# Kernel optimization log

Hardware: AMD Instinct MI355X
Metric: run time of the kernel (lower is better)

## Reference

```python
import jax, jax.numpy as jnp
import numpy as np

K = 3       # attractive nearest neighbors
J = 3       # repulsive offset (uses dist[:, :, J:])
ALPHA = 0.1
NU = 1e-3


def setup_inputs() -> dict:
    key = jax.random.key(0)
    k1, k2 = jax.random.split(key, 2)
    phi_p = jax.random.normal(k1, (4, 512, 64, 64), dtype=jnp.float32)
    memory_bank = jax.random.normal(k2, (16384, 512), dtype=jnp.float32)
    r = jnp.ones((1,), dtype=jnp.float32)
    return {"phi_p": phi_p, "memory_bank": memory_bank, "r": r}


def reference(phi_p, memory_bank, r):
    B, C, H, W = phi_p.shape
    # b c h w -> b (h w) c
    x = phi_p.reshape(B, C, H * W).transpose(0, 2, 1)
    x2 = jnp.sum(x * x, axis=-1, keepdims=True)            # [B, HW, 1]
    m2 = jnp.sum(memory_bank * memory_bank, axis=-1)       # [N]
    d2 = x2 + m2[None, None, :] - 2.0 * jnp.einsum('bnc,mc->bnm', x, memory_bank)
    d2 = jnp.maximum(d2, 0.0)                              # [B, HW, N]
    # smallest K+J squared distances, ascending (topk(largest=False))
    neg_top, _ = jax.lax.top_k(-d2, K + J)
    dist = -neg_top                                        # [B, HW, K+J]
    r2 = r ** 2
    scores_att = dist[:, :, :K] - r2
    loss_att = jnp.mean(jnp.maximum(scores_att, 0.0)) / NU
    scores_rep = r2 - dist[:, :, J:] - ALPHA
    loss_rep = jnp.mean(jnp.maximum(scores_rep, 0.0)) / NU
    return loss_att + loss_rep
```

## Files before the change

kernel.cpp:

```cpp
#include <hip/hip_runtime.h>
#include <cfloat>

#define B_   4
#define C_   512
#define HW_  4096
#define R_   16384
#define N_   16384
#define ALPHA_ 0.1f
#define SCALE_ ((float)(1000.0/49152.0))

typedef unsigned int u32;
typedef unsigned short u16;
typedef unsigned char u8;
typedef __attribute__((ext_vector_type(2))) unsigned long long u64x2;
typedef __attribute__((ext_vector_type(4))) float f32x4;

typedef const __attribute__((address_space(1))) u32* gas_u32;
typedef __attribute__((address_space(3))) u32* las_u32;

__device__ __forceinline__ void async16(const void* g, void* l) {
    __builtin_amdgcn_global_load_lds((gas_u32)g, (las_u32)l, 16, 0, 0);
}

__device__ __forceinline__ u32 pk_fp8x4(float a, float b, float c, float d) {
    u32 v = __builtin_amdgcn_cvt_pk_fp8_f32(a, b, 0, false);
    v = __builtin_amdgcn_cvt_pk_fp8_f32(c, d, v, true);
    return v;
}

__device__ __forceinline__ void ins6(float (&t)[6], float v) {
    if (v < t[5]) {
        t[5] = v;
        #pragma unroll
        for (int q = 5; q >= 1; --q) {
            float lo = fminf(t[q-1], t[q]);
            float hi = fmaxf(t[q-1], t[q]);
            t[q-1] = lo; t[q] = hi;
        }
    }
}

__global__ void conv_mem_kernel(const float* __restrict__ mem,
                                u8* __restrict__ Mb, float* __restrict__ m2) {
    int w = threadIdx.x >> 6, l = threadIdx.x & 63;
    int row = blockIdx.x * 4 + w;
    const float4* p = (const float4*)(mem + (size_t)row * C_);
    float4 a = p[l], b = p[l + 64];
    float s = a.x*a.x + a.y*a.y + a.z*a.z + a.w*a.w
            + b.x*b.x + b.y*b.y + b.z*b.z + b.w*b.w;
    *(u32*)(Mb + (size_t)row * C_ + l*4)       = pk_fp8x4(a.x, a.y, a.z, a.w);
    *(u32*)(Mb + (size_t)row * C_ + 256 + l*4) = pk_fp8x4(b.x, b.y, b.z, b.w);
    #pragma unroll
    for (int off = 32; off > 0; off >>= 1) s += __shfl_down(s, off);
    if (l == 0) m2[row] = s;
}

__global__ void conv_phi_kernel(const float* __restrict__ phi, u8* __restrict__ Xb,
                                float* __restrict__ x2) {
    __shared__ float T[64][65];
    int t = threadIdx.x;
    int n0 = blockIdx.x * 64, c0 = blockIdx.y * 64, b = blockIdx.z;
    const float* src = phi + ((size_t)b * C_ + c0) * HW_ + n0;
    int l = t & 63, cg = t >> 6;
    float sq = 0.f;
    #pragma unroll
    for (int p = 0; p < 16; ++p) {
        int c = cg + p * 4;
        float v = src[(size_t)c * HW_ + l];
        T[c][l] = v;
        sq = fmaf(v, v, sq);
    }
    atomicAdd(&x2[(size_t)b * HW_ + n0 + l], sq);
    __syncthreads();
    int cq = t & 15, gl0 = t >> 4;
    #pragma unroll
    for (int p = 0; p < 4; ++p) {
        int gl = gl0 + p * 16;
        u32 v = pk_fp8x4(T[cq*4+0][gl], T[cq*4+1][gl],
                         T[cq*4+2][gl], T[cq*4+3][gl]);
        size_t g = (size_t)b * HW_ + n0 + gl;
        *(u32*)(Xb + g * C_ + c0 + cq*4) = v;
    }
}

template<int NC>
__global__ __launch_bounds__(256, 3) void gemm_topk_kernel(
    const u8* __restrict__ Xb, const u8* __restrict__ Mb,
    const float* __restrict__ m2, float* __restrict__ P ) {
    __shared__ __align__(16) u8 smem[32768];
    const int t = threadIdx.x;
    const int w = t >> 6, l = t & 63;
    const int g0  = blockIdx.x * 64;
    const int n0c = blockIdx.y * (N_ / NC);
    const int mband = w * 32;
    const int fm  = l & 15;
    const int rq  = l >> 4;
    const int pc  = (rq ^ ((fm >> 1) & 3)) * 16;
    const int srow4 = l >> 2;
    const int soff  = (((l & 3) ^ ((l >> 3) & 3)) * 16);

    u64x2 ax[4][2];
    {
        const u8* Xr = Xb + (size_t)(g0 + w*16 + fm) * C_ + rq * 16;
        #pragma unroll
        for (int s = 0; s < 4; ++s) {
            ax[s][0] = *(const u64x2*)(Xr + s*128);
            ax[s][1] = *(const u64x2*)(Xr + s*128 + 64);
        }
    }

    float top[4][6];
    #pragma unroll
    for (int s4 = 0; s4 < 4; ++s4)
        #pragma unroll
        for (int q = 0; q < 6; ++q) top[s4][q] = FLT_MAX;

    {
        const u8* Msrc = Mb + (size_t)(n0c + mband) * C_;
        #pragma unroll
        for (int h = 0; h < 2; ++h)
            #pragma unroll
            for (int i = 0; i < 2; ++i)
                async16(Msrc + (size_t)(i*16 + srow4) * C_ + h*64 + soff,
                        smem + mband*64 + h*8192 + i*1024);
    }
    __syncthreads();

    const int NT = N_ / NC / 128;
    #pragma unroll 1
    for (int nt = 0; nt < NT; ++nt) {
        const int n0 = n0c + nt * 128;

        f32x4 acc[8];
        #pragma unroll
        for (int n = 0; n < 8; ++n) acc[n] = (f32x4)0.f;

        #pragma unroll
        for (int s = 0; s < 4; ++s) {
            {
                const int nt2 = (s == 3) ? nt + 1 : nt;
                const int s2  = (s + 1) & 3;
                if (nt2 < NT) {
                    const u8* Msrc = Mb + (size_t)(n0c + nt2*128 + mband) * C_ + s2*128;
                    u8* dst = smem + ((s+1)&1)*16384 + mband*64;
                    #pragma unroll
                    for (int h = 0; h < 2; ++h)
                        #pragma unroll
                        for (int i = 0; i < 2; ++i)
                            async16(Msrc + (size_t)(i*16 + srow4) * C_ + h*64 + soff,
                                    dst + h*8192 + i*1024);
                }
            }
            const u8* bufp = smem + (s&1)*16384;
            #pragma unroll
            for (int h = 0; h < 2; ++h) {
                const u8* Mh = bufp + h * 8192;
                const u64x2 a = ax[s][h];
                #pragma unroll
                for (int n = 0; n < 8; ++n) {
                    u64x2 bv = *(const u64x2*)(Mh + (n*16 + fm) * 64 + pc);
                    acc[n] = __builtin_amdgcn_mfma_f32_16x16x32_fp8_fp8(
                        (long)a.x, (long)bv.x, acc[n], 0, 0, 0);
                    acc[n] = __builtin_amdgcn_mfma_f32_16x16x32_fp8_fp8(
                        (long)a.y, (long)bv.y, acc[n], 0, 0, 0);
                }
            }

            if (s == 3) {
                float m2w[8];
                #pragma unroll
                for (int n = 0; n < 8; ++n) m2w[n] = m2[n0 + n * 16 + fm];
                #pragma unroll
                for (int j = 0; j < 4; ++j) {
                    float d0 = m2w[0] - 2.f * acc[0][j];
                    float d1 = m2w[1] - 2.f * acc[1][j];
                    float d2 = m2w[2] - 2.f * acc[2][j];
                    float d3 = m2w[3] - 2.f * acc[3][j];
                    float d4 = m2w[4] - 2.f * acc[4][j];
                    float d5 = m2w[5] - 2.f * acc[5][j];
                    float d6 = m2w[6] - 2.f * acc[6][j];
                    float d7 = m2w[7] - 2.f * acc[7][j];
                    float vmin = fminf(fminf(fminf(d0, d1), fminf(d2, d3)),
                                       fminf(fminf(d4, d5), fminf(d6, d7)));
                    float (&tt)[6] = top[j];
                    if (vmin < tt[5]) {
                        ins6(tt, d0); ins6(tt, d1); ins6(tt, d2); ins6(tt, d3);
                        ins6(tt, d4); ins6(tt, d5); ins6(tt, d6); ins6(tt, d7);
                    }
                }
            }
            __syncthreads();
        }
    }

    float* Mg = (float*)smem;
    #pragma unroll
    for (int j = 0; j < 4; ++j) {
        int lrow = w * 16 + rq * 4 + j;
        #pragma unroll
        for (int q = 0; q < 6; ++q)
            Mg[lrow * 97 + fm * 6 + q] = top[j][q];
    }
    __syncthreads();
    if (t < 64) {
        float t6[6];
        #pragma unroll
        for (int q = 0; q < 6; ++q) t6[q] = FLT_MAX;
        const float* row = Mg + t * 97;
        for (int v = 0; v < 96; ++v) ins6(t6, row[v]);
        float* dst = P + ((size_t)(g0 + t) * NC + blockIdx.y) * 6;
        #pragma unroll
        for (int q = 0; q < 6; ++q) dst[q] = t6[q];
    }
}

template<int NC>
__global__ void finalize_kernel(const float* __restrict__ P, const float* __restrict__ x2,
                                const float* __restrict__ rp, float* __restrict__ out) {
    int g = blockIdx.x * 256 + threadIdx.x;
    float t6[6];
    #pragma unroll
    for (int q = 0; q < 6; ++q) t6[q] = FLT_MAX;
    const f32x4* pp = (const f32x4*)(P + (size_t)g * (NC * 6));
    #pragma unroll
    for (int q = 0; q < NC * 6 / 4; ++q) {
        f32x4 v = pp[q];
        ins6(t6, v.x); ins6(t6, v.y); ins6(t6, v.z); ins6(t6, v.w);
    }
    float x2g = x2[g];
    float rv = rp[0], r2 = rv * rv;
    float s = 0.f;
    #pragma unroll
    for (int i = 0; i < 3; ++i) {
        float d = fmaxf(t6[i] + x2g, 0.f);
        s += fmaxf(d - r2, 0.f);
    }
    #pragma unroll
    for (int i = 3; i < 6; ++i) {
        float d = fmaxf(t6[i] + x2g, 0.f);
        s += fmaxf(r2 - d - ALPHA_, 0.f);
    }
    #pragma unroll
    for (int off = 32; off > 0; off >>= 1) s += __shfl_down(s, off);
    __shared__ float red[4];
    int w = threadIdx.x >> 6, l = threadIdx.x & 63;
    if (l == 0) red[w] = s;
    __syncthreads();
    if (threadIdx.x == 0)
        atomicAdd(out, (red[0] + red[1] + red[2] + red[3]) * SCALE_);
}

#define TM 64
#define TN 64
#define KC 64
#define LDP 68

__global__ void m2_kernel(const float* __restrict__ mem, float* __restrict__ m2) {
    int wave = threadIdx.x >> 6, lane = threadIdx.x & 63;
    int row = blockIdx.x * 4 + wave;
    const float4* p = reinterpret_cast<const float4*>(mem + (size_t)row * C_);
    float4 a = p[lane], b = p[lane + 64];
    float s = a.x*a.x + a.y*a.y + a.z*a.z + a.w*a.w
            + b.x*b.x + b.y*b.y + b.z*b.z + b.w*b.w;
    #pragma unroll
    for (int off = 32; off > 0; off >>= 1) s += __shfl_down(s, off);
    if (lane == 0) m2[row] = s;
}

__global__ void x2f_kernel(const float* __restrict__ phi, float* __restrict__ x2) {
    int g = blockIdx.x * blockDim.x + threadIdx.x;
    int b = g >> 12;
    int n = g & 4095;
    const float* p = phi + (size_t)b * C_ * HW_ + n;
    float s = 0.f;
    #pragma unroll 8
    for (int c = 0; c < C_; ++c) {
        float v = p[(size_t)c * HW_];
        s = fmaf(v, v, s);
    }
    x2[g] = s;
}

__global__ __launch_bounds__(256) void dist_loss_kernel(
    const float* __restrict__ phi, const float* __restrict__ mem,
    const float* __restrict__ rp,  const float* __restrict__ m2,
    const float* __restrict__ x2,  float* __restrict__ out) {
    __shared__ float smem[2 * TM * LDP];
    float* xs = smem;
    float* ms = smem + TM * LDP;
    const int tid = threadIdx.x;
    const int tx = tid & 15, ty = tid >> 4;
    const int g0 = blockIdx.x * TM;
    const int b = g0 >> 12, n0img = g0 & 4095;
    const float* phiB = phi + (size_t)b * C_ * HW_ + n0img;
    float top[4][6];
    #pragma unroll
    for (int i = 0; i < 4; ++i)
        #pragma unroll
        for (int q = 0; q < 6; ++q) top[i][q] = FLT_MAX;
    float x2v[4];
    #pragma unroll
    for (int i = 0; i < 4; ++i) x2v[i] = x2[g0 + ty * 4 + i];
    for (int nt = 0; nt < N_ / TN; ++nt) {
        const int n0 = nt * TN;
        float acc[4][4];
        #pragma unroll
        for (int i = 0; i < 4; ++i)
            #pragma unroll
            for (int j = 0; j < 4; ++j) acc[i][j] = 0.f;
        for (int s = 0; s < C_ / KC; ++s) {
            const int k0 = s * KC;
            {
                int rr = tid & 63, cb = tid >> 6;
                #pragma unroll
                for (int p = 0; p < 16; ++p) {
                    int cc = p * 4 + cb;
                    xs[rr * LDP + cc] = phiB[(size_t)(k0 + cc) * HW_ + rr];
                }
            }
            {
                int kq = tid & 15, cb = tid >> 4;
                #pragma unroll
                for (int p = 0; p < 4; ++p) {
                    int c = p * 16 + cb;
                    float4 v = *reinterpret_cast<const float4*>(
                        mem + (size_t)(n0 + c) * C_ + k0 + kq * 4);
                    ms[(kq*4+0)*LDP + c] = v.x; ms[(kq*4+1)*LDP + c] = v.y;
                    ms[(kq*4+2)*LDP + c] = v.z; ms[(kq*4+3)*LDP + c] = v.w;
                }
            }
            __syncthreads();
            #pragma unroll
            for (int kq = 0; kq < KC / 4; ++kq) {
                float4 xa[4], mb[4];
                #pragma unroll
                for (int i = 0; i < 4; ++i)
                    xa[i] = *reinterpret_cast<const float4*>(&xs[(ty*4+i)*LDP + kq*4]);
                #pragma unroll
                for (int kk = 0; kk < 4; ++kk)
                    mb[kk] = *reinterpret_cast<const float4*>(&ms[(kq*4+kk)*LDP + tx*4]);
                #pragma unroll
                for (int i = 0; i < 4; ++i) {
                    const float xk[4] = {xa[i].x, xa[i].y, xa[i].z, xa[i].w};
                    #pragma unroll
                    for (int kk = 0; kk < 4; ++kk) {
                        const float mc[4] = {mb[kk].x, mb[kk].y, mb[kk].z, mb[kk].w};
                        #pragma unroll
                        for (int j = 0; j < 4; ++j)
                            acc[i][j] = fmaf(xk[kk], mc[j], acc[i][j]);
                    }
                }
            }
            __syncthreads();
        }
        #pragma unroll
        for (int j = 0; j < 4; ++j) {
            float m2v = m2[n0 + tx * 4 + j];
            #pragma unroll
            for (int i = 0; i < 4; ++i) {
                float d = fmaxf(x2v[i] + m2v - 2.f * acc[i][j], 0.f);
                ins6(top[i], d);
            }
        }
    }
    __syncthreads();
    float* mg = smem;
    #pragma unroll
    for (int i = 0; i < 4; ++i)
        #pragma unroll
        for (int q = 0; q < 6; ++q)
            mg[(ty*4+i)*97 + tx*6 + q] = top[i][q];
    __syncthreads();
    if (tid < 64) {
        float t6[6];
        #pragma unroll
        for (int q = 0; q < 6; ++q) t6[q] = FLT_MAX;
        const float* row = mg + tid * 97;
        for (int v = 0; v < 96; ++v) ins6(t6, row[v]);
        float rv = rp[0], r2 = rv * rv;
        float s = fmaxf(t6[0]-r2,0.f) + fmaxf(t6[1]-r2,0.f) + fmaxf(t6[2]-r2,0.f)
                + fmaxf(r2-t6[3]-ALPHA_,0.f) + fmaxf(r2-t6[4]-ALPHA_,0.f)
                + fmaxf(r2-t6[5]-ALPHA_,0.f);
        #pragma unroll
        for (int off = 32; off > 0; off >>= 1) s += __shfl_down(s, off);
        if (tid == 0) atomicAdd(out, s * SCALE_);
    }
}

extern "C" void kernel_launch(void* const* d_in, const int* in_sizes, int n_in,
                              void* d_out, int out_size, void* d_ws, size_t ws_size,
                              hipStream_t stream) {
    const float* phi = (const float*)d_in[0];
    const float* mem = (const float*)d_in[1];
    const float* rp  = (const float*)d_in[2];
    float* out = (float*)d_out;

    const size_t offX  = 0;
    const size_t offM  = (size_t)R_ * C_;
    const size_t offx2 = offM + (size_t)N_ * C_;
    const size_t offm2 = offx2 + (size_t)R_ * 4;
    const size_t offP  = offm2 + (size_t)N_ * 4;
    const size_t need8 = offP + (size_t)R_ * 8 * 6 * 4;
    const size_t need4 = offP + (size_t)R_ * 4 * 6 * 4;

    hipMemsetAsync(out, 0, sizeof(float), stream);

    if (ws_size >= need4) {
        u8*    Xb = (u8*)((char*)d_ws + offX);
        u8*    Mb = (u8*)((char*)d_ws + offM);
        float* x2 = (float*)((char*)d_ws + offx2);
        float* m2 = (float*)((char*)d_ws + offm2);
        float* P  = (float*)((char*)d_ws + offP);

        hipMemsetAsync(x2, 0, (size_t)R_ * 4, stream);
        conv_mem_kernel<<<N_ / 4, 256, 0, stream>>>(mem, Mb, m2);
        conv_phi_kernel<<<dim3(HW_ / 64, C_ / 64, B_), 256, 0, stream>>>(phi, Xb, x2);
        if (ws_size >= need8) {
            gemm_topk_kernel<8><<<dim3(R_ / 64, 8), 256, 0, stream>>>(Xb, Mb, m2, P);
            finalize_kernel<8><<<R_ / 256, 256, 0, stream>>>(P, x2, rp, out);
        } else {
            gemm_topk_kernel<4><<<dim3(R_ / 64, 4), 256, 0, stream>>>(Xb, Mb, m2, P);
            finalize_kernel<4><<<R_ / 256, 256, 0, stream>>>(P, x2, rp, out);
        }
    } else {
        float* m2 = (float*)d_ws;
        float* x2 = m2 + N_;
        m2_kernel<<<N_ / 4, 256, 0, stream>>>(mem, m2);
        x2f_kernel<<<R_ / 256, 256, 0, stream>>>(phi, x2);
        dist_loss_kernel<<<R_ / TM, 256, 0, stream>>>(phi, mem, rp, m2, x2, out);
    }
}
```

Measured before the change: 351.8 us.

## Split B tile between LDS staging and direct global loads, use 4-way N split

Only half of each 128-column memory-bank tile (columns 0-63) is now staged in LDS through async global-to-LDS copies. The other half (columns 64-127) is loaded straight from global memory into registers for each k-slice, which halves LDS traffic and the double-buffer footprint. The launch also always uses the 4-way split over N, dropping the 8-way variant. The direct loads are uncoalesced 16-byte rows repeated across the four waves, which adds L2/global traffic and register pressure, and the 4-way split yields fewer blocks.

```diff
diff --git a/kernel.cpp b/kernel.cpp
--- a/kernel.cpp
+++ b/kernel.cpp
@@ -92,7 +92,7 @@
     const int w = t >> 6, l = t & 63;
     const int g0  = blockIdx.x * 64;
     const int n0c = blockIdx.y * (N_ / NC);
-    const int mband = w * 32;
+    const int mband = w * 16;
     const int fm  = l & 15;
     const int rq  = l >> 4;
     const int pc  = (rq ^ ((fm >> 1) & 3)) * 16;
@@ -116,13 +116,10 @@
         for (int q = 0; q < 6; ++q) top[s4][q] = FLT_MAX;
 
     {
-        const u8* Msrc = Mb + (size_t)(n0c + mband) * C_;
-        #pragma unroll
-        for (int h = 0; h < 2; ++h)
-            #pragma unroll
-            for (int i = 0; i < 2; ++i)
-                async16(Msrc + (size_t)(i*16 + srow4) * C_ + h*64 + soff,
-                        smem + mband*64 + h*8192 + i*1024);
+        const u8* Msrc = Mb + (size_t)(n0c + mband + srow4) * C_;
+        u8* dst = smem + mband * 64;
+        async16(Msrc + soff,      dst);
+        async16(Msrc + 64 + soff, dst + 4096);
     }
     __syncthreads();
 
@@ -137,33 +134,60 @@
 
         #pragma unroll
         for (int s = 0; s < 4; ++s) {
+            const int k0 = s * 128;
+            u64x2 bg0h0, bg0h1, bg1h0, bg1h1, bg2h0, bg2h1, bg3h0, bg3h1;
+            {
+                const u8* Mr0 = Mb + (size_t)(n0 + 4*16 + fm) * C_ + k0 + rq*16;
+                const u8* Mr1 = Mb + (size_t)(n0 + 5*16 + fm) * C_ + k0 + rq*16;
+                const u8* Mr2 = Mb + (size_t)(n0 + 6*16 + fm) * C_ + k0 + rq*16;
+                const u8* Mr3 = Mb + (size_t)(n0 + 7*16 + fm) * C_ + k0 + rq*16;
+                bg0h0 = *(const u64x2*)(Mr0);  bg0h1 = *(const u64x2*)(Mr0 + 64);
+                bg1h0 = *(const u64x2*)(Mr1);  bg1h1 = *(const u64x2*)(Mr1 + 64);
+                bg2h0 = *(const u64x2*)(Mr2);  bg2h1 = *(const u64x2*)(Mr2 + 64);
+                bg3h0 = *(const u64x2*)(Mr3);  bg3h1 = *(const u64x2*)(Mr3 + 64);
+            }
             {
                 const int nt2 = (s == 3) ? nt + 1 : nt;
                 const int s2  = (s + 1) & 3;
                 if (nt2 < NT) {
-                    const u8* Msrc = Mb + (size_t)(n0c + nt2*128 + mband) * C_ + s2*128;
-                    u8* dst = smem + ((s+1)&1)*16384 + mband*64;
-                    #pragma unroll
-                    for (int h = 0; h < 2; ++h)
-                        #pragma unroll
-                        for (int i = 0; i < 2; ++i)
-                            async16(Msrc + (size_t)(i*16 + srow4) * C_ + h*64 + soff,
-                                    dst + h*8192 + i*1024);
-                }
-            }
-            const u8* bufp = smem + (s&1)*16384;
+                    const u8* Msrc = Mb + (size_t)(n0c + nt2*128 + mband + srow4) * C_
+                                        + s2*128;
+                    u8* dst = smem + ((s+1)&1)*8192 + mband*64;
+                    async16(Msrc + soff,      dst);
+                    async16(Msrc + 64 + soff, dst + 4096);
+                }
+            }
+            const u8* bufp = smem + (s&1)*8192;
             #pragma unroll
             for (int h = 0; h < 2; ++h) {
-                const u8* Mh = bufp + h * 8192;
                 const u64x2 a = ax[s][h];
                 #pragma unroll
-                for (int n = 0; n < 8; ++n) {
-                    u64x2 bv = *(const u64x2*)(Mh + (n*16 + fm) * 64 + pc);
+                for (int n = 0; n < 4; ++n) {
+                    u64x2 bv = *(const u64x2*)(bufp + h*4096 + (n*16 + fm) * 64 + pc);
                     acc[n] = __builtin_amdgcn_mfma_f32_16x16x32_fp8_fp8(
                         (long)a.x, (long)bv.x, acc[n], 0, 0, 0);
                     acc[n] = __builtin_amdgcn_mfma_f32_16x16x32_fp8_fp8(
                         (long)a.y, (long)bv.y, acc[n], 0, 0, 0);
                 }
+            }
+            {
+                const u64x2 a0 = ax[s][0], a1 = ax[s][1];
+                acc[4] = __builtin_amdgcn_mfma_f32_16x16x32_fp8_fp8((long)a0.x, (long)bg0h0.x, acc[4], 0, 0, 0);
+                acc[5] = __builtin_amdgcn_mfma_f32_16x16x32_fp8_fp8((long)a0.x, (long)bg1h0.x, acc[5], 0, 0, 0);
+                acc[6] = __builtin_amdgcn_mfma_f32_16x16x32_fp8_fp8((long)a0.x, (long)bg2h0.x, acc[6], 0, 0, 0);
+                acc[7] = __builtin_amdgcn_mfma_f32_16x16x32_fp8_fp8((long)a0.x, (long)bg3h0.x, acc[7], 0, 0, 0);
+                acc[4] = __builtin_amdgcn_mfma_f32_16x16x32_fp8_fp8((long)a0.y, (long)bg0h0.y, acc[4], 0, 0, 0);
+                acc[5] = __builtin_amdgcn_mfma_f32_16x16x32_fp8_fp8((long)a0.y, (long)bg1h0.y, acc[5], 0, 0, 0);
+                acc[6] = __builtin_amdgcn_mfma_f32_16x16x32_fp8_fp8((long)a0.y, (long)bg2h0.y, acc[6], 0, 0, 0);
+                acc[7] = __builtin_amdgcn_mfma_f32_16x16x32_fp8_fp8((long)a0.y, (long)bg3h0.y, acc[7], 0, 0, 0);
+                acc[4] = __builtin_amdgcn_mfma_f32_16x16x32_fp8_fp8((long)a1.x, (long)bg0h1.x, acc[4], 0, 0, 0);
+                acc[5] = __builtin_amdgcn_mfma_f32_16x16x32_fp8_fp8((long)a1.x, (long)bg1h1.x, acc[5], 0, 0, 0);
+                acc[6] = __builtin_amdgcn_mfma_f32_16x16x32_fp8_fp8((long)a1.x, (long)bg2h1.x, acc[6], 0, 0, 0);
+                acc[7] = __builtin_amdgcn_mfma_f32_16x16x32_fp8_fp8((long)a1.x, (long)bg3h1.x, acc[7], 0, 0, 0);
+                acc[4] = __builtin_amdgcn_mfma_f32_16x16x32_fp8_fp8((long)a1.y, (long)bg0h1.y, acc[4], 0, 0, 0);
+                acc[5] = __builtin_amdgcn_mfma_f32_16x16x32_fp8_fp8((long)a1.y, (long)bg1h1.y, acc[5], 0, 0, 0);
+                acc[6] = __builtin_amdgcn_mfma_f32_16x16x32_fp8_fp8((long)a1.y, (long)bg2h1.y, acc[6], 0, 0, 0);
+                acc[7] = __builtin_amdgcn_mfma_f32_16x16x32_fp8_fp8((long)a1.y, (long)bg3h1.y, acc[7], 0, 0, 0);
             }
 
             if (s == 3) {
@@ -400,7 +424,6 @@
     const size_t offx2 = offM + (size_t)N_ * C_;
     const size_t offm2 = offx2 + (size_t)R_ * 4;
     const size_t offP  = offm2 + (size_t)N_ * 4;
-    const size_t need8 = offP + (size_t)R_ * 8 * 6 * 4;
     const size_t need4 = offP + (size_t)R_ * 4 * 6 * 4;
 
     hipMemsetAsync(out, 0, sizeof(float), stream);
@@ -415,13 +438,8 @@
         hipMemsetAsync(x2, 0, (size_t)R_ * 4, stream);
         conv_mem_kernel<<<N_ / 4, 256, 0, stream>>>(mem, Mb, m2);
         conv_phi_kernel<<<dim3(HW_ / 64, C_ / 64, B_), 256, 0, stream>>>(phi, Xb, x2);
-        if (ws_size >= need8) {
-            gemm_topk_kernel<8><<<dim3(R_ / 64, 8), 256, 0, stream>>>(Xb, Mb, m2, P);
-            finalize_kernel<8><<<R_ / 256, 256, 0, stream>>>(P, x2, rp, out);
-        } else {
-            gemm_topk_kernel<4><<<dim3(R_ / 64, 4), 256, 0, stream>>>(Xb, Mb, m2, P);
-            finalize_kernel<4><<<R_ / 256, 256, 0, stream>>>(P, x2, rp, out);
-        }
+        gemm_topk_kernel<4><<<dim3(R_ / 64, 4), 256, 0, stream>>>(Xb, Mb, m2, P);
+        finalize_kernel<4><<<R_ / 256, 256, 0, stream>>>(P, x2, rp, out);
     } else {
         float* m2 = (float*)d_ws;
         float* x2 = m2 + N_;
```

Measured after the change: 719.6 us. 105% more time.
